# Performance work log

Hardware: AMD Instinct MI355X
Metric: run time of the kernel (lower is better)

The kernel has to match this reference:

```python
import jax, jax.numpy as jnp
import numpy as np
from jax import lax

NUM_KERNELS = 256
B, C, L = 128, 10, 16384
EPS = 1e-10
NORMALIZE = True
KERNEL_LENGTHS = np.array([7, 9, 11])


def _make_kernel_meta():
    """Deterministic ROCKET-style ragged kernel metadata (static ints)."""
    rng = np.random.default_rng(0)
    lengths = rng.choice(KERNEL_LENGTHS, NUM_KERNELS).astype(np.int64)
    nci = rng.integers(1, C + 1, NUM_KERNELS).astype(np.int64)  # channels per kernel
    channel_indices = np.concatenate(
        [rng.choice(C, int(n), replace=False) for n in nci]).astype(np.int64)
    dilations = np.array(
        [int(2 ** rng.uniform(0.0, np.log2((L - 1) / (l - 1)))) for l in lengths],
        dtype=np.int64)
    paddings = np.array(
        [((l - 1) * d) // 2 if rng.integers(2) else 0 for l, d in zip(lengths, dilations)],
        dtype=np.int64)
    return lengths, nci, channel_indices, dilations, paddings


def setup_inputs() -> dict:
    lengths, nci, channel_indices, dilations, paddings = _make_kernel_meta()
    total_w = int(np.sum(lengths * nci))
    key = jax.random.key(0)
    kx, kw, kb = jax.random.split(key, 3)
    x = jax.random.normal(kx, (B, C, L), dtype=jnp.float32)
    weights = jax.random.normal(kw, (total_w,), dtype=jnp.float32)
    biases = jax.random.uniform(kb, (NUM_KERNELS,), minval=-1.0, maxval=1.0,
                                dtype=jnp.float32)
    return {
        'x': x,
        'weights': weights,
        'biases': biases,
        'lengths': jnp.asarray(lengths),
        'dilations': jnp.asarray(dilations),
        'paddings': jnp.asarray(paddings),
        'num_channel_indices': jnp.asarray(nci),
        'channel_indices': jnp.asarray(channel_indices),
    }


def reference(x, weights, biases, lengths, dilations, paddings,
              num_channel_indices, channel_indices):
    # Ragged metadata must be static (defines per-kernel shapes).
    lengths = np.asarray(lengths)
    dilations = np.asarray(dilations)
    paddings = np.asarray(paddings)
    nci = np.asarray(num_channel_indices)
    channel_indices = np.asarray(channel_indices)
    windices = np.concatenate([[0], np.cumsum(lengths * nci)])
    cindices = np.concatenate([[0], np.cumsum(nci)])

    if NORMALIZE:
        mean_ = jnp.mean(x, axis=-1, keepdims=True)
        std_ = jnp.std(x, axis=-1, keepdims=True, ddof=1)  # torch unbiased std
        x = (x - mean_) / (std_ + EPS)

    ppvs, mxs = [], []
    for k in range(NUM_KERNELS):
        w = weights[windices[k]:windices[k + 1]].reshape(int(nci[k]), int(lengths[k]))
        chans = channel_indices[cindices[k]:cindices[k + 1]]
        px = x[:, chans, :]                       # [B, c_k, L]
        d, p = int(dilations[k]), int(paddings[k])
        yy = lax.conv_general_dilated(
            px, w[None],                          # rhs: [1, c_k, len_k]
            window_strides=(1,), padding=[(p, p)], rhs_dilation=(d,),
            dimension_numbers=('NCH', 'OIH', 'NCH'))[:, 0, :] + biases[k]  # [B, Lout]
        ppvs.append(jnp.mean((yy > 0).astype(x.dtype), axis=-1))
        sm = jax.nn.softmax(yy * 1000.0, axis=-1)  # sharp softmax ~ smooth max
        mxs.append(jnp.sum(sm * yy, axis=-1))

    ppv = jnp.stack(ppvs, axis=1)                 # [B, K]
    mx = jnp.stack(mxs, axis=1)                   # [B, K]
    # interleave: y[:, 2k] = ppv_k, y[:, 2k+1] = mx_k
    return jnp.stack([ppv, mx], axis=2).reshape(x.shape[0], 2 * NUM_KERNELS)
```

## Files before the change

### kernel.cpp

```cpp
#include <hip/hip_runtime.h>

#define NK 256
#define BB 128
#define CC 10
#define LL 16384
#define EPSV 1e-10f
#define GS2 15
#define XW 1792
#define WROW 12

__device__ __forceinline__ void block_finish(int cnt, float mx,
                                             float* rm, int* rc,
                                             int Lout, float* out, int b, int k) {
    int tid = threadIdx.x;
    for (int off = 32; off; off >>= 1) {
        mx = fmaxf(mx, __shfl_down(mx, off));
        cnt += __shfl_down(cnt, off);
    }
    int wv = tid >> 6, ln = tid & 63;
    if (ln == 0) { rm[wv] = mx; rc[wv] = cnt; }
    __syncthreads();
    if (tid == 0) {
#pragma unroll
        for (int i = 1; i < 4; ++i) { mx = fmaxf(mx, rm[i]); cnt += rc[i]; }
        size_t o = (size_t)b * (2 * NK) + 2 * k;
        out[o] = (float)cnt / (float)Lout;
        out[o + 1] = mx;
    }
}

__global__ __launch_bounds__(256) void stats_kernel(const float* __restrict__ x,
                                                    float* __restrict__ wsf) {
    int row = blockIdx.x;
    const float4* x4 = (const float4*)(x + (size_t)row * LL);
    int tid = threadIdx.x;
    float s = 0.f, s2 = 0.f;
    for (int i = tid; i < LL / 4; i += 256) {
        float4 v = x4[i];
        s += v.x + v.y + v.z + v.w;
        s2 += v.x * v.x + v.y * v.y + v.z * v.z + v.w * v.w;
    }
    for (int off = 32; off; off >>= 1) {
        s += __shfl_down(s, off);
        s2 += __shfl_down(s2, off);
    }
    __shared__ float as_[4], as2_[4];
    int wv = tid >> 6, ln = tid & 63;
    if (ln == 0) { as_[wv] = s; as2_[wv] = s2; }
    __syncthreads();
    if (tid == 0) {
        float S = as_[0] + as_[1] + as_[2] + as_[3];
        float S2 = as2_[0] + as2_[1] + as2_[2] + as2_[3];
        float mean = S / (float)LL;
        float var = (S2 - (float)LL * mean * mean) / (float)(LL - 1);
        var = fmaxf(var, 0.f);
        float inv = 1.f / (sqrtf(var) + EPSV);
        wsf[row] = inv;
        wsf[1280 + row] = -mean * inv;
    }
}

__global__ __launch_bounds__(256) void prefix_kernel(const int* __restrict__ lengths,
                                                     const int* __restrict__ ncis,
                                                     int* __restrict__ wbase,
                                                     int* __restrict__ cbase) {
    __shared__ int s1[NK], s2[NK];
    int k = threadIdx.x;
    int v1 = lengths[k] * ncis[k];
    int v2 = ncis[k];
    s1[k] = v1; s2[k] = v2;
    for (int off = 1; off < NK; off <<= 1) {
        __syncthreads();
        int a = (k >= off) ? s1[k - off] : 0;
        int b = (k >= off) ? s2[k - off] : 0;
        __syncthreads();
        s1[k] += a; s2[k] += b;
    }
    __syncthreads();
    wbase[k] = s1[k] - v1;
    cbase[k] = s2[k] - v2;
}

template <int LEN>
__device__ __forceinline__ void conv_S(
    const float* __restrict__ x, float* __restrict__ xw,
    const float* __restrict__ wsmR, const float* __restrict__ wsmS,
    const int* __restrict__ choff, const float* __restrict__ cinv,
    const float* __restrict__ csh,
    int d, int ms, int Lout, int nci, float biasE, float biasI,
    int wu, int lane, int& cnt, float& mx) {
    constexpr int W = GS2 + LEN - 1;
    const int qpt = 64 / d;
    const int MT = qpt * GS2;
    const int stot = d * (MT + LEN - 1);
    const int nit4 = (stot + 3 + 255) >> 8;
    const int nitS = (stot + 3 + 63) >> 6;
    const int Qmax = (Lout + d - 1) / d;
    const int nqt = (Qmax + MT - 1) / MT;
    int qi = lane / d, rho = lane - qi * d;
    bool act = qi < qpt;
    int a0 = act ? qi * GS2 * d + rho : 0;
    float rv[28];

    for (int j = wu; j < nqt; j += 4) {
        int qt = j * MT;
        int tb = (qt - ms) * d;
        int off = tb & 3, base = tb - off;
        bool interior = (base >= 0) && (base + (nit4 << 8) <= LL);
        float acc[GS2];
#pragma unroll
        for (int g = 0; g < GS2; ++g) acc[g] = 0.f;

        if (interior) {
            {
                const float* xp = x + choff[0] + base + 4 * lane;
#pragma unroll
                for (int it = 0; it < 7; ++it)
                    if (it < nit4) *(float4*)&rv[4 * it] = *(const float4*)(xp + (it << 8));
            }
            for (int ci = 0; ci < nci; ++ci) {
#pragma unroll
                for (int it = 0; it < 7; ++it)
                    if (it < nit4) *(float4*)&xw[4 * lane + (it << 8)] = *(const float4*)&rv[4 * it];
                if (ci + 1 < nci) {
                    const float* xp = x + choff[ci + 1] + base + 4 * lane;
#pragma unroll
                    for (int it = 0; it < 7; ++it)
                        if (it < nit4) *(float4*)&rv[4 * it] = *(const float4*)(xp + (it << 8));
                }
                float wreg[WROW];
                const float4* wv4 = (const float4*)&wsmS[ci * WROW];
#pragma unroll
                for (int u = 0; u < (LEN + 3) / 4; ++u) {
                    float4 w4 = wv4[u];
                    wreg[4 * u + 0] = w4.x; wreg[4 * u + 1] = w4.y;
                    wreg[4 * u + 2] = w4.z; wreg[4 * u + 3] = w4.w;
                }
                float win[W];
                int a = off + a0;
#pragma unroll
                for (int i = 0; i < W; ++i) { win[i] = xw[a]; a += d; }
                __builtin_amdgcn_s_setprio(1);
#pragma unroll
                for (int jj = 0; jj < LEN; ++jj)
#pragma unroll
                    for (int g = 0; g < GS2; ++g)
                        acc[g] = fmaf(wreg[jj], win[g + jj], acc[g]);
                __builtin_amdgcn_s_setprio(0);
            }
        } else {
            {
                const float* xc = x + choff[0];
#pragma unroll
                for (int it = 0; it < 26; ++it)
                    if (it < nitS) {
                        int t = base + (it << 6) + lane;
                        t = t < 0 ? 0 : (t > LL - 1 ? LL - 1 : t);
                        rv[it] = xc[t];
                    }
            }
            for (int ci = 0; ci < nci; ++ci) {
                float inv = cinv[ci], sh = csh[ci];
#pragma unroll
                for (int it = 0; it < 26; ++it)
                    if (it < nitS) {
                        int t = base + (it << 6) + lane;
                        float v = ((unsigned)t < (unsigned)LL) ? fmaf(rv[it], inv, sh) : 0.f;
                        xw[(it << 6) + lane] = v;
                    }
                if (ci + 1 < nci) {
                    const float* xc = x + choff[ci + 1];
#pragma unroll
                    for (int it = 0; it < 26; ++it)
                        if (it < nitS) {
                            int t = base + (it << 6) + lane;
                            t = t < 0 ? 0 : (t > LL - 1 ? LL - 1 : t);
                            rv[it] = xc[t];
                        }
                }
                float wreg[WROW];
                const float4* wv4 = (const float4*)&wsmR[ci * WROW];
#pragma unroll
                for (int u = 0; u < (LEN + 3) / 4; ++u) {
                    float4 w4 = wv4[u];
                    wreg[4 * u + 0] = w4.x; wreg[4 * u + 1] = w4.y;
                    wreg[4 * u + 2] = w4.z; wreg[4 * u + 3] = w4.w;
                }
                float win[W];
                int a = off + a0;
#pragma unroll
                for (int i = 0; i < W; ++i) { win[i] = xw[a]; a += d; }
                __builtin_amdgcn_s_setprio(1);
#pragma unroll
                for (int jj = 0; jj < LEN; ++jj)
#pragma unroll
                    for (int g = 0; g < GS2; ++g)
                        acc[g] = fmaf(wreg[jj], win[g + jj], acc[g]);
                __builtin_amdgcn_s_setprio(0);
            }
        }

        float bt = interior ? biasI : biasE;
        if (act) {
            int qb = qt + qi * GS2;
            if ((qb + GS2) * d <= Lout) {
                float am = acc[0];
#pragma unroll
                for (int g = 1; g < GS2; ++g) am = fmaxf(am, acc[g]);
                mx = fmaxf(mx, am + bt);
                float nb = -bt;
#pragma unroll
                for (int g = 0; g < GS2; ++g) cnt += (acc[g] > nb) ? 1 : 0;
            } else {
#pragma unroll
                for (int g = 0; g < GS2; ++g) {
                    int t = (qb + g) * d + rho;
                    if (t < Lout) {
                        float y = acc[g] + bt;
                        cnt += (y > 0.f) ? 1 : 0;
                        mx = fmaxf(mx, y);
                    }
                }
            }
        }
    }
}

template <int LEN, int GG>
__device__ __forceinline__ void conv_T(
    const float* __restrict__ x,
    const float* __restrict__ wsmR, const float* __restrict__ wsmS,
    const int* __restrict__ choff, const float* __restrict__ cinv,
    const float* __restrict__ csh,
    int d, int ms, int Lout, int nci, float biasE, float biasI,
    int wu, int lane, int& cnt, float& mx) {
    constexpr int M = GG + LEN - 1;
    const int Qmax = (Lout + d - 1) / d;
    const int nqt = (Qmax + GG - 1) / GG;
    const int NT = d * nqt;

    for (int f0 = wu * 64; f0 < NT; f0 += 256) {
        int f = f0 + lane;
        bool active = f < NT;
        int fc = active ? f : NT - 1;
        unsigned qi = (unsigned)fc / (unsigned)d;
        int rho = fc - (int)qi * d;
        int qb0 = (int)qi * GG;
        int tl = (qb0 - ms) * d + rho;
        bool laneInt = (tl >= 0) && (tl + (M - 1) * d < LL);
        bool interior = __all(laneInt);
        float acc[GG];
#pragma unroll
        for (int g = 0; g < GG; ++g) acc[g] = 0.f;

        float rA[M], rB[M];

        if (interior) {
            {
                const float* xc = x + choff[0];
                int t = tl;
#pragma unroll
                for (int m = 0; m < M; ++m) { rA[m] = xc[t]; t += d; }
            }
            int ci = 0;
            while (true) {
                if (ci + 1 < nci) {
                    const float* xc = x + choff[ci + 1];
                    int t = tl;
#pragma unroll
                    for (int m = 0; m < M; ++m) { rB[m] = xc[t]; t += d; }
                }
                {
                    float wreg[WROW];
                    const float4* wv4 = (const float4*)&wsmS[ci * WROW];
#pragma unroll
                    for (int u = 0; u < (LEN + 3) / 4; ++u) {
                        float4 w4 = wv4[u];
                        wreg[4 * u + 0] = w4.x; wreg[4 * u + 1] = w4.y;
                        wreg[4 * u + 2] = w4.z; wreg[4 * u + 3] = w4.w;
                    }
                    __builtin_amdgcn_s_setprio(1);
#pragma unroll
                    for (int jj = 0; jj < LEN; ++jj)
#pragma unroll
                        for (int g = 0; g < GG; ++g)
                            acc[g] = fmaf(wreg[jj], rA[g + jj], acc[g]);
                    __builtin_amdgcn_s_setprio(0);
                }
                ++ci; if (ci >= nci) break;
                if (ci + 1 < nci) {
                    const float* xc = x + choff[ci + 1];
                    int t = tl;
#pragma unroll
                    for (int m = 0; m < M; ++m) { rA[m] = xc[t]; t += d; }
                }
                {
                    float wreg[WROW];
                    const float4* wv4 = (const float4*)&wsmS[ci * WROW];
#pragma unroll
                    for (int u = 0; u < (LEN + 3) / 4; ++u) {
                        float4 w4 = wv4[u];
                        wreg[4 * u + 0] = w4.x; wreg[4 * u + 1] = w4.y;
                        wreg[4 * u + 2] = w4.z; wreg[4 * u + 3] = w4.w;
                    }
                    __builtin_amdgcn_s_setprio(1);
#pragma unroll
                    for (int jj = 0; jj < LEN; ++jj)
#pragma unroll
                        for (int g = 0; g < GG; ++g)
                            acc[g] = fmaf(wreg[jj], rB[g + jj], acc[g]);
                    __builtin_amdgcn_s_setprio(0);
                }
                ++ci; if (ci >= nci) break;
            }
        } else {
            {
                const float* xc = x + choff[0];
                int t = tl;
#pragma unroll
                for (int m = 0; m < M; ++m) {
                    int tc = t < 0 ? 0 : (t > LL - 1 ? LL - 1 : t);
                    rA[m] = xc[tc]; t += d;
                }
            }
            int ci = 0;
            while (true) {
                if (ci + 1 < nci) {
                    const float* xc = x + choff[ci + 1];
                    int t = tl;
#pragma unroll
                    for (int m = 0; m < M; ++m) {
                        int tc = t < 0 ? 0 : (t > LL - 1 ? LL - 1 : t);
                        rB[m] = xc[tc]; t += d;
                    }
                }
                {
                    float inv = cinv[ci], sh = csh[ci];
                    int t = tl;
#pragma unroll
                    for (int m = 0; m < M; ++m) {
                        rA[m] = ((unsigned)t < (unsigned)LL) ? fmaf(rA[m], inv, sh) : 0.f;
                        t += d;
                    }
                    float wreg[WROW];
                    const float4* wv4 = (const float4*)&wsmR[ci * WROW];
#pragma unroll
                    for (int u = 0; u < (LEN + 3) / 4; ++u) {
                        float4 w4 = wv4[u];
                        wreg[4 * u + 0] = w4.x; wreg[4 * u + 1] = w4.y;
                        wreg[4 * u + 2] = w4.z; wreg[4 * u + 3] = w4.w;
                    }
                    __builtin_amdgcn_s_setprio(1);
#pragma unroll
                    for (int jj = 0; jj < LEN; ++jj)
#pragma unroll
                        for (int g = 0; g < GG; ++g)
                            acc[g] = fmaf(wreg[jj], rA[g + jj], acc[g]);
                    __builtin_amdgcn_s_setprio(0);
                }
                ++ci; if (ci >= nci) break;
                if (ci + 1 < nci) {
                    const float* xc = x + choff[ci + 1];
                    int t = tl;
#pragma unroll
                    for (int m = 0; m < M; ++m) {
                        int tc = t < 0 ? 0 : (t > LL - 1 ? LL - 1 : t);
                        rA[m] = xc[tc]; t += d;
                    }
                }
                {
                    float inv = cinv[ci], sh = csh[ci];
                    int t = tl;
#pragma unroll
                    for (int m = 0; m < M; ++m) {
                        rB[m] = ((unsigned)t < (unsigned)LL) ? fmaf(rB[m], inv, sh) : 0.f;
                        t += d;
                    }
                    float wreg[WROW];
                    const float4* wv4 = (const float4*)&wsmR[ci * WROW];
#pragma unroll
                    for (int u = 0; u < (LEN + 3) / 4; ++u) {
                        float4 w4 = wv4[u];
                        wreg[4 * u + 0] = w4.x; wreg[4 * u + 1] = w4.y;
                        wreg[4 * u + 2] = w4.z; wreg[4 * u + 3] = w4.w;
                    }
                    __builtin_amdgcn_s_setprio(1);
#pragma unroll
                    for (int jj = 0; jj < LEN; ++jj)
#pragma unroll
                        for (int g = 0; g < GG; ++g)
                            acc[g] = fmaf(wreg[jj], rB[g + jj], acc[g]);
                    __builtin_amdgcn_s_setprio(0);
                }
                ++ci; if (ci >= nci) break;
            }
        }

        float bt = interior ? biasI : biasE;
        if (active) {
            if ((qb0 + GG) * d <= Lout) {
                float am = acc[0];
#pragma unroll
                for (int g = 1; g < GG; ++g) am = fmaxf(am, acc[g]);
                mx = fmaxf(mx, am + bt);
                float nb = -bt;
#pragma unroll
                for (int g = 0; g < GG; ++g) cnt += (acc[g] > nb) ? 1 : 0;
            } else {
#pragma unroll
                for (int g = 0; g < GG; ++g) {
                    int t = (qb0 + g) * d + rho;
                    if (t < Lout) {
                        float y = acc[g] + bt;
                        cnt += (y > 0.f) ? 1 : 0;
                        mx = fmaxf(mx, y);
                    }
                }
            }
        }
    }
}

__global__ __launch_bounds__(256) void conv_kernel(
    const float* __restrict__ x, const float* __restrict__ weights,
    const float* __restrict__ biases,
    const int* __restrict__ lengths, const int* __restrict__ dil,
    const int* __restrict__ pad, const int* __restrict__ ncis,
    const int* __restrict__ chidx,
    const float* __restrict__ wsf, const int* __restrict__ wbase,
    const int* __restrict__ cbase, float* __restrict__ out) {
    int k = blockIdx.x, b = blockIdx.y;
    __shared__ __align__(16) float xl[4 * XW];
    __shared__ __align__(16) float wsmR[CC * WROW];
    __shared__ __align__(16) float wsmS[CC * WROW];
    __shared__ int choff[CC];
    __shared__ float cinv[CC], csh[CC];
    __shared__ float rm[4];
    __shared__ int rc[4];

    int tid = threadIdx.x;
    int len = lengths[k], d = dil[k], p = pad[k], nci = ncis[k];
    int wb = wbase[k], cb = cbase[k];

    if (tid < nci) {
        int ch = chidx[cb + tid];
        choff[tid] = (b * CC + ch) * LL;
        cinv[tid] = wsf[b * CC + ch];
        csh[tid] = wsf[1280 + b * CC + ch];
    }
    __syncthreads();
    for (int i = tid; i < nci * WROW; i += 256) {
        int ci = i / WROW, jj = i - ci * WROW;
        float wv = (jj < len) ? weights[wb + ci * len + jj] : 0.f;
        wsmR[i] = wv;
        wsmS[i] = wv * cinv[ci];
    }
    __syncthreads();

    float csum = 0.f;
    for (int ci = 0; ci < nci; ++ci) {
        float sw = 0.f;
        for (int jj = 0; jj < WROW; ++jj) sw += wsmR[ci * WROW + jj];
        csum += csh[ci] * sw;
    }

    int span = (len - 1) * d;
    int Lout = LL + 2 * p - span;
    int ms = p / d;
    float biasE = biases[k];
    float biasI = biasE + csum;
    int Qmax = (Lout + d - 1) / d;

    int wu = tid >> 6;
    int lane = tid & 63;
    float* xw = xl + wu * XW;
    int cnt = 0;
    float mx = -3.4e38f;

    if (d <= 16) {
        switch (len) {
            case 7:  conv_S<7>(x, xw, wsmR, wsmS, choff, cinv, csh, d, ms, Lout, nci, biasE, biasI, wu, lane, cnt, mx); break;
            case 9:  conv_S<9>(x, xw, wsmR, wsmS, choff, cinv, csh, d, ms, Lout, nci, biasE, biasI, wu, lane, cnt, mx); break;
            default: conv_S<11>(x, xw, wsmR, wsmS, choff, cinv, csh, d, ms, Lout, nci, biasE, biasI, wu, lane, cnt, mx); break;
        }
    } else if (Qmax > 12) {
        switch (len) {
            case 7:  conv_T<7, 16>(x, wsmR, wsmS, choff, cinv, csh, d, ms, Lout, nci, biasE, biasI, wu, lane, cnt, mx); break;
            case 9:  conv_T<9, 16>(x, wsmR, wsmS, choff, cinv, csh, d, ms, Lout, nci, biasE, biasI, wu, lane, cnt, mx); break;
            default: conv_T<11, 16>(x, wsmR, wsmS, choff, cinv, csh, d, ms, Lout, nci, biasE, biasI, wu, lane, cnt, mx); break;
        }
    } else {
        switch (len) {
            case 7:  conv_T<7, 4>(x, wsmR, wsmS, choff, cinv, csh, d, ms, Lout, nci, biasE, biasI, wu, lane, cnt, mx); break;
            case 9:  conv_T<9, 4>(x, wsmR, wsmS, choff, cinv, csh, d, ms, Lout, nci, biasE, biasI, wu, lane, cnt, mx); break;
            default: conv_T<11, 4>(x, wsmR, wsmS, choff, cinv, csh, d, ms, Lout, nci, biasE, biasI, wu, lane, cnt, mx); break;
        }
    }
    block_finish(cnt, mx, rm, rc, Lout, out, b, k);
}

extern "C" void kernel_launch(void* const* d_in, const int* in_sizes, int n_in,
                              void* d_out, int out_size, void* d_ws, size_t ws_size,
                              hipStream_t stream) {
    const float* x = (const float*)d_in[0];
    const float* weights = (const float*)d_in[1];
    const float* biases = (const float*)d_in[2];
    const int* lengths = (const int*)d_in[3];
    const int* dil = (const int*)d_in[4];
    const int* pad = (const int*)d_in[5];
    const int* ncis = (const int*)d_in[6];
    const int* chidx = (const int*)d_in[7];
    float* out = (float*)d_out;

    float* wsf = (float*)d_ws;
    int* wbase = (int*)((char*)d_ws + 2560 * sizeof(float));
    int* cbase = wbase + NK;

    stats_kernel<<<dim3(BB * CC), dim3(256), 0, stream>>>(x, wsf);
    prefix_kernel<<<dim3(1), dim3(256), 0, stream>>>(lengths, ncis, wbase, cbase);
    dim3 grid(NK, BB);
    conv_kernel<<<grid, dim3(256), 0, stream>>>(x, weights, biases, lengths, dil,
                                                pad, ncis, chidx, wsf, wbase,
                                                cbase, out);
}
```

Baseline: 2.213 ms.

## Sort kernels by work for scheduling, specialize small-dilation conv on dilation, shrink LDS

The prefix kernel now ranks the 256 ROCKET kernels by estimated work (channels times output positions per phase) and writes a permutation, so the conv grid launches the heaviest kernels first to reduce tail imbalance. The small-dilation conv path is templated on the dilation value (1..16) through a switch, which makes loop trip counts, register array sizes and strides compile-time constants. The per-wave LDS window is reduced from 1792 to 1280 floats, which may allow more blocks per CU. Costs are much larger code size from 48 instantiations, and a risk that the smaller window no longer fits the largest tile.

```diff
diff --git a/kernel.cpp b/kernel.cpp
--- a/kernel.cpp
+++ b/kernel.cpp
@@ -6,7 +6,7 @@
 #define LL 16384
 #define EPSV 1e-10f
 #define GS2 15
-#define XW 1792
+#define XW 1280
 #define WROW 12
 
 __device__ __forceinline__ void block_finish(int cnt, float mx,
@@ -62,12 +62,20 @@
 
 __global__ __launch_bounds__(256) void prefix_kernel(const int* __restrict__ lengths,
                                                      const int* __restrict__ ncis,
+                                                     const int* __restrict__ dil,
+                                                     const int* __restrict__ pad,
                                                      int* __restrict__ wbase,
-                                                     int* __restrict__ cbase) {
-    __shared__ int s1[NK], s2[NK];
+                                                     int* __restrict__ cbase,
+                                                     int* __restrict__ perm) {
+    __shared__ int s1[NK], s2[NK], swk[NK];
     int k = threadIdx.x;
-    int v1 = lengths[k] * ncis[k];
+    int len = lengths[k], d = dil[k], p = pad[k];
+    int v1 = len * ncis[k];
     int v2 = ncis[k];
+    int Lout = LL + 2 * p - (len - 1) * d;
+    int Qmax = (Lout + d - 1) / d;
+    int wk = v2 * Qmax;
+    swk[k] = wk;
     s1[k] = v1; s2[k] = v2;
     for (int off = 1; off < NK; off <<= 1) {
         __syncthreads();
@@ -79,151 +87,171 @@
     __syncthreads();
     wbase[k] = s1[k] - v1;
     cbase[k] = s2[k] - v2;
+    int rank = 0;
+    for (int j = 0; j < NK; ++j) {
+        int wj = swk[j];
+        rank += (wj > wk) || (wj == wk && j < k) ? 1 : 0;
+    }
+    perm[rank] = k;
+}
+
+template <int LEN, int D>
+__device__ __forceinline__ void conv_S(
+    const float* __restrict__ x, float* __restrict__ xw,
+    const float* __restrict__ wsmR, const float* __restrict__ wsmS,
+    const int* __restrict__ choff, const float* __restrict__ cinv,
+    const float* __restrict__ csh,
+    int ms, int Lout, int nci, float biasE, float biasI,
+    int wu, int lane, int& cnt, float& mx) {
+    constexpr int W = GS2 + LEN - 1;
+    constexpr int qpt = 64 / D;
+    constexpr int MT = qpt * GS2;
+    constexpr int stot = D * (MT + LEN - 1);
+    constexpr int nit4 = (stot + 3 + 255) >> 8;
+    constexpr int nitS = (stot + 3 + 63) >> 6;
+    constexpr int RVN = (4 * nit4 > nitS) ? 4 * nit4 : nitS;
+    const int Qmax = (Lout + D - 1) / D;
+    const int nqt = (Qmax + MT - 1) / MT;
+    int qi = lane / D, rho = lane - qi * D;
+    bool act = qi < qpt;
+    int a0 = act ? qi * GS2 * D + rho : 0;
+    float rv[RVN];
+
+    for (int j = wu; j < nqt; j += 4) {
+        int qt = j * MT;
+        int tb = (qt - ms) * D;
+        int off = tb & 3, base = tb - off;
+        bool interior = (base >= 0) && (base + (nit4 << 8) <= LL);
+        float acc[GS2];
+#pragma unroll
+        for (int g = 0; g < GS2; ++g) acc[g] = 0.f;
+
+        if (interior) {
+            {
+                const float* xp = x + choff[0] + base + 4 * lane;
+#pragma unroll
+                for (int it = 0; it < nit4; ++it)
+                    *(float4*)&rv[4 * it] = *(const float4*)(xp + (it << 8));
+            }
+            for (int ci = 0; ci < nci; ++ci) {
+#pragma unroll
+                for (int it = 0; it < nit4; ++it)
+                    *(float4*)&xw[4 * lane + (it << 8)] = *(const float4*)&rv[4 * it];
+                if (ci + 1 < nci) {
+                    const float* xp = x + choff[ci + 1] + base + 4 * lane;
+#pragma unroll
+                    for (int it = 0; it < nit4; ++it)
+                        *(float4*)&rv[4 * it] = *(const float4*)(xp + (it << 8));
+                }
+                float wreg[WROW];
+                const float4* wv4 = (const float4*)&wsmS[ci * WROW];
+#pragma unroll
+                for (int u = 0; u < (LEN + 3) / 4; ++u) {
+                    float4 w4 = wv4[u];
+                    wreg[4 * u + 0] = w4.x; wreg[4 * u + 1] = w4.y;
+                    wreg[4 * u + 2] = w4.z; wreg[4 * u + 3] = w4.w;
+                }
+                float win[W];
+                int ab = off + a0;
+#pragma unroll
+                for (int i = 0; i < W; ++i) win[i] = xw[ab + i * D];
+                __builtin_amdgcn_s_setprio(1);
+#pragma unroll
+                for (int jj = 0; jj < LEN; ++jj)
+#pragma unroll
+                    for (int g = 0; g < GS2; ++g)
+                        acc[g] = fmaf(wreg[jj], win[g + jj], acc[g]);
+                __builtin_amdgcn_s_setprio(0);
+            }
+        } else {
+            {
+                const float* xc = x + choff[0];
+#pragma unroll
+                for (int it = 0; it < nitS; ++it) {
+                    int t = base + (it << 6) + lane;
+                    t = t < 0 ? 0 : (t > LL - 1 ? LL - 1 : t);
+                    rv[it] = xc[t];
+                }
+            }
+            for (int ci = 0; ci < nci; ++ci) {
+                float inv = cinv[ci], sh = csh[ci];
+#pragma unroll
+                for (int it = 0; it < nitS; ++it) {
+                    int t = base + (it << 6) + lane;
+                    float v = ((unsigned)t < (unsigned)LL) ? fmaf(rv[it], inv, sh) : 0.f;
+                    xw[(it << 6) + lane] = v;
+                }
+                if (ci + 1 < nci) {
+                    const float* xc = x + choff[ci + 1];
+#pragma unroll
+                    for (int it = 0; it < nitS; ++it) {
+                        int t = base + (it << 6) + lane;
+                        t = t < 0 ? 0 : (t > LL - 1 ? LL - 1 : t);
+                        rv[it] = xc[t];
+                    }
+                }
+                float wreg[WROW];
+                const float4* wv4 = (const float4*)&wsmR[ci * WROW];
+#pragma unroll
+                for (int u = 0; u < (LEN + 3) / 4; ++u) {
+                    float4 w4 = wv4[u];
+                    wreg[4 * u + 0] = w4.x; wreg[4 * u + 1] = w4.y;
+                    wreg[4 * u + 2] = w4.z; wreg[4 * u + 3] = w4.w;
+                }
+                float win[W];
+                int ab = off + a0;
+#pragma unroll
+                for (int i = 0; i < W; ++i) win[i] = xw[ab + i * D];
+                __builtin_amdgcn_s_setprio(1);
+#pragma unroll
+                for (int jj = 0; jj < LEN; ++jj)
+#pragma unroll
+                    for (int g = 0; g < GS2; ++g)
+                        acc[g] = fmaf(wreg[jj], win[g + jj], acc[g]);
+                __builtin_amdgcn_s_setprio(0);
+            }
+        }
+
+        float bt = interior ? biasI : biasE;
+        if (act) {
+            int qb = qt + qi * GS2;
+            if ((qb + GS2) * D <= Lout) {
+                float am = acc[0];
+#pragma unroll
+                for (int g = 1; g < GS2; ++g) am = fmaxf(am, acc[g]);
+                mx = fmaxf(mx, am + bt);
+                float nb = -bt;
+#pragma unroll
+                for (int g = 0; g < GS2; ++g) cnt += (acc[g] > nb) ? 1 : 0;
+            } else {
+#pragma unroll
+                for (int g = 0; g < GS2; ++g) {
+                    int t = (qb + g) * D + rho;
+                    if (t < Lout) {
+                        float y = acc[g] + bt;
+                        cnt += (y > 0.f) ? 1 : 0;
+                        mx = fmaxf(mx, y);
+                    }
+                }
+            }
+        }
+    }
 }
 
 template <int LEN>
-__device__ __forceinline__ void conv_S(
+__device__ __forceinline__ void conv_S_d(
     const float* __restrict__ x, float* __restrict__ xw,
     const float* __restrict__ wsmR, const float* __restrict__ wsmS,
     const int* __restrict__ choff, const float* __restrict__ cinv,
     const float* __restrict__ csh,
     int d, int ms, int Lout, int nci, float biasE, float biasI,
     int wu, int lane, int& cnt, float& mx) {
-    constexpr int W = GS2 + LEN - 1;
-    const int qpt = 64 / d;
-    const int MT = qpt * GS2;
-    const int stot = d * (MT + LEN - 1);
-    const int nit4 = (stot + 3 + 255) >> 8;
-    const int nitS = (stot + 3 + 63) >> 6;
-    const int Qmax = (Lout + d - 1) / d;
-    const int nqt = (Qmax + MT - 1) / MT;
-    int qi = lane / d, rho = lane - qi * d;
-    bool act = qi < qpt;
-    int a0 = act ? qi * GS2 * d + rho : 0;
-    float rv[28];
-
-    for (int j = wu; j < nqt; j += 4) {
-        int qt = j * MT;
-        int tb = (qt - ms) * d;
-        int off = tb & 3, base = tb - off;
-        bool interior = (base >= 0) && (base + (nit4 << 8) <= LL);
-        float acc[GS2];
-#pragma unroll
-        for (int g = 0; g < GS2; ++g) acc[g] = 0.f;
-
-        if (interior) {
-            {
-                const float* xp = x + choff[0] + base + 4 * lane;
-#pragma unroll
-                for (int it = 0; it < 7; ++it)
-                    if (it < nit4) *(float4*)&rv[4 * it] = *(const float4*)(xp + (it << 8));
-            }
-            for (int ci = 0; ci < nci; ++ci) {
-#pragma unroll
-                for (int it = 0; it < 7; ++it)
-                    if (it < nit4) *(float4*)&xw[4 * lane + (it << 8)] = *(const float4*)&rv[4 * it];
-                if (ci + 1 < nci) {
-                    const float* xp = x + choff[ci + 1] + base + 4 * lane;
-#pragma unroll
-                    for (int it = 0; it < 7; ++it)
-                        if (it < nit4) *(float4*)&rv[4 * it] = *(const float4*)(xp + (it << 8));
-                }
-                float wreg[WROW];
-                const float4* wv4 = (const float4*)&wsmS[ci * WROW];
-#pragma unroll
-                for (int u = 0; u < (LEN + 3) / 4; ++u) {
-                    float4 w4 = wv4[u];
-                    wreg[4 * u + 0] = w4.x; wreg[4 * u + 1] = w4.y;
-                    wreg[4 * u + 2] = w4.z; wreg[4 * u + 3] = w4.w;
-                }
-                float win[W];
-                int a = off + a0;
-#pragma unroll
-                for (int i = 0; i < W; ++i) { win[i] = xw[a]; a += d; }
-                __builtin_amdgcn_s_setprio(1);
-#pragma unroll
-                for (int jj = 0; jj < LEN; ++jj)
-#pragma unroll
-                    for (int g = 0; g < GS2; ++g)
-                        acc[g] = fmaf(wreg[jj], win[g + jj], acc[g]);
-                __builtin_amdgcn_s_setprio(0);
-            }
-        } else {
-            {
-                const float* xc = x + choff[0];
-#pragma unroll
-                for (int it = 0; it < 26; ++it)
-                    if (it < nitS) {
-                        int t = base + (it << 6) + lane;
-                        t = t < 0 ? 0 : (t > LL - 1 ? LL - 1 : t);
-                        rv[it] = xc[t];
-                    }
-            }
-            for (int ci = 0; ci < nci; ++ci) {
-                float inv = cinv[ci], sh = csh[ci];
-#pragma unroll
-                for (int it = 0; it < 26; ++it)
-                    if (it < nitS) {
-                        int t = base + (it << 6) + lane;
-                        float v = ((unsigned)t < (unsigned)LL) ? fmaf(rv[it], inv, sh) : 0.f;
-                        xw[(it << 6) + lane] = v;
-                    }
-                if (ci + 1 < nci) {
-                    const float* xc = x + choff[ci + 1];
-#pragma unroll
-                    for (int it = 0; it < 26; ++it)
-                        if (it < nitS) {
-                            int t = base + (it << 6) + lane;
-                            t = t < 0 ? 0 : (t > LL - 1 ? LL - 1 : t);
-                            rv[it] = xc[t];
-                        }
-                }
-                float wreg[WROW];
-                const float4* wv4 = (const float4*)&wsmR[ci * WROW];
-#pragma unroll
-                for (int u = 0; u < (LEN + 3) / 4; ++u) {
-                    float4 w4 = wv4[u];
-                    wreg[4 * u + 0] = w4.x; wreg[4 * u + 1] = w4.y;
-                    wreg[4 * u + 2] = w4.z; wreg[4 * u + 3] = w4.w;
-                }
-                float win[W];
-                int a = off + a0;
-#pragma unroll
-                for (int i = 0; i < W; ++i) { win[i] = xw[a]; a += d; }
-                __builtin_amdgcn_s_setprio(1);
-#pragma unroll
-                for (int jj = 0; jj < LEN; ++jj)
-#pragma unroll
-                    for (int g = 0; g < GS2; ++g)
-                        acc[g] = fmaf(wreg[jj], win[g + jj], acc[g]);
-                __builtin_amdgcn_s_setprio(0);
-            }
-        }
-
-        float bt = interior ? biasI : biasE;
-        if (act) {
-            int qb = qt + qi * GS2;
-            if ((qb + GS2) * d <= Lout) {
-                float am = acc[0];
-#pragma unroll
-                for (int g = 1; g < GS2; ++g) am = fmaxf(am, acc[g]);
-                mx = fmaxf(mx, am + bt);
-                float nb = -bt;
-#pragma unroll
-                for (int g = 0; g < GS2; ++g) cnt += (acc[g] > nb) ? 1 : 0;
-            } else {
-#pragma unroll
-                for (int g = 0; g < GS2; ++g) {
-                    int t = (qb + g) * d + rho;
-                    if (t < Lout) {
-                        float y = acc[g] + bt;
-                        cnt += (y > 0.f) ? 1 : 0;
-                        mx = fmaxf(mx, y);
-                    }
-                }
-            }
-        }
-    }
+#define SC(DD) case DD: conv_S<LEN, DD>(x, xw, wsmR, wsmS, choff, cinv, csh, ms, Lout, nci, biasE, biasI, wu, lane, cnt, mx); break;
+    switch (d) {
+        SC(1) SC(2) SC(3) SC(4) SC(5) SC(6) SC(7) SC(8)
+        SC(9) SC(10) SC(11) SC(12) SC(13) SC(14) SC(15) SC(16)
+    }
+#undef SC
 }
 
 template <int LEN, int GG>
@@ -428,8 +456,10 @@
     const int* __restrict__ pad, const int* __restrict__ ncis,
     const int* __restrict__ chidx,
     const float* __restrict__ wsf, const int* __restrict__ wbase,
-    const int* __restrict__ cbase, float* __restrict__ out) {
-    int k = blockIdx.x, b = blockIdx.y;
+    const int* __restrict__ cbase, const int* __restrict__ perm,
+    float* __restrict__ out) {
+    int k = perm[blockIdx.x];
+    int b = blockIdx.y;
     __shared__ __align__(16) float xl[4 * XW];
     __shared__ __align__(16) float wsmR[CC * WROW];
     __shared__ __align__(16) float wsmS[CC * WROW];
@@ -479,9 +509,9 @@
 
     if (d <= 16) {
         switch (len) {
-            case 7:  conv_S<7>(x, xw, wsmR, wsmS, choff, cinv, csh, d, ms, Lout, nci, biasE, biasI, wu, lane, cnt, mx); break;
-            case 9:  conv_S<9>(x, xw, wsmR, wsmS, choff, cinv, csh, d, ms, Lout, nci, biasE, biasI, wu, lane, cnt, mx); break;
-            default: conv_S<11>(x, xw, wsmR, wsmS, choff, cinv, csh, d, ms, Lout, nci, biasE, biasI, wu, lane, cnt, mx); break;
+            case 7:  conv_S_d<7>(x, xw, wsmR, wsmS, choff, cinv, csh, d, ms, Lout, nci, biasE, biasI, wu, lane, cnt, mx); break;
+            case 9:  conv_S_d<9>(x, xw, wsmR, wsmS, choff, cinv, csh, d, ms, Lout, nci, biasE, biasI, wu, lane, cnt, mx); break;
+            default: conv_S_d<11>(x, xw, wsmR, wsmS, choff, cinv, csh, d, ms, Lout, nci, biasE, biasI, wu, lane, cnt, mx); break;
         }
     } else if (Qmax > 12) {
         switch (len) {
@@ -515,11 +545,13 @@
     float* wsf = (float*)d_ws;
     int* wbase = (int*)((char*)d_ws + 2560 * sizeof(float));
     int* cbase = wbase + NK;
+    int* perm = cbase + NK;
 
     stats_kernel<<<dim3(BB * CC), dim3(256), 0, stream>>>(x, wsf);
-    prefix_kernel<<<dim3(1), dim3(256), 0, stream>>>(lengths, ncis, wbase, cbase);
+    prefix_kernel<<<dim3(1), dim3(256), 0, stream>>>(lengths, ncis, dil, pad,
+                                                     wbase, cbase, perm);
     dim3 grid(NK, BB);
     conv_kernel<<<grid, dim3(256), 0, stream>>>(x, weights, biases, lengths, dil,
                                                 pad, ncis, chidx, wsf, wbase,
-                                                cbase, out);
-}
+                                                cbase, perm, out);
+}
```

After: 1.888 ms (median of 2 runs). 1.17x faster.
